# Kernel tuning notes

Hardware: AMD Instinct MI355X
Metric: run time of the kernel (lower is better)

The kernel has to match this reference:

```python
import jax, jax.numpy as jnp
import numpy as np

B, P = 4, 2048
N = B * P
QD = 512            # query_dim == inner_dim (pos_emb is added to raw features)
CD = 512            # context_dim
HEADS, DH = 8, 64
INNER = HEADS * DH
SCALE = DH ** -0.5
HC, WC = 32, 32     # context spatial grid
L = HC * WC         # context_len
SELF_HW = 512       # spatial_dim[:2]
STRIDE = 8          # resolution_level == sparse tensor stride
PE_H = SELF_HW // STRIDE  # 64 BEV pos-emb grid


def setup_inputs() -> dict:
    key = jax.random.key(0)
    k = jax.random.split(key, 9)
    return {
        "feats": jax.random.normal(k[0], (N, QD), jnp.float32),
        "coords_xy": jax.random.randint(k[1], (N, 2), 0, SELF_HW),
        "context_emb": jax.random.normal(k[2], (B, HC, WC, CD), jnp.float32),
        "Wq": jax.random.normal(k[3], (QD, INNER), jnp.float32) * 0.02,
        "Wk": jax.random.normal(k[4], (CD, INNER), jnp.float32) * 0.02,
        "Wv": jax.random.normal(k[5], (CD, INNER), jnp.float32) * 0.02,
        "Wo": jax.random.normal(k[6], (INNER, QD), jnp.float32) * 0.02,
        "bo": jnp.zeros((QD,), jnp.float32),
        "pos_embedding": jax.random.normal(k[7], (PE_H, PE_H, INNER), jnp.float32) / INNER ** 0.5,
        "context_pos_embedding": jax.random.normal(k[8], (L, CD), jnp.float32) / INNER ** 0.5,
    }


def _neighbor_mask(coords_xy):
    # get_context_mask: scatter a (2*STRIDE+1)^2 neighborhood around each point's
    # projected context cell into a [N, L] boolean mask
    ratio = jnp.float32(HC) / jnp.float32(SELF_HW)
    center = jnp.round(coords_xy.astype(jnp.float32) * ratio).astype(jnp.int32)  # [N,2]
    off = jnp.stack(
        jnp.meshgrid(jnp.arange(-STRIDE, STRIDE + 1), jnp.arange(-STRIDE, STRIDE + 1), indexing="ij"),
        axis=-1,
    ).reshape(-1, 2)  # [K,2], K = 289
    pos = center[:, None, :] + off[None, :, :]        # [N,K,2]
    r = jnp.clip(pos[..., 0], 0, HC - 1)
    c = jnp.clip(pos[..., 1], 0, WC - 1)
    flat = r * WC + c                                  # [N,K]
    return jnp.zeros((N, L), jnp.bool_).at[jnp.arange(N)[:, None], flat].set(True)


def reference(feats, coords_xy, context_emb, Wq, Wk, Wv, Wo, bo, pos_embedding, context_pos_embedding):
    # get_context: add learned context positional embedding, flatten spatial -> [B, L, CD]
    ctx = (context_emb + context_pos_embedding.reshape(HC, WC, CD)).reshape(B, L, CD)
    # get_pos_emb: gather BEV positional embedding per point via floor(coord/stride)
    rc = coords_xy // STRIDE                           # [N,2] in [0, 64)
    pe = pos_embedding[rc[:, 0], rc[:, 1]]             # [N, INNER]
    f = (feats + pe).reshape(B, P, QD)                 # points grouped per batch (equal counts)
    mask = _neighbor_mask(coords_xy).reshape(B, P, L)
    q = (f @ Wq).reshape(B, P, HEADS, DH).transpose(0, 2, 1, 3)    # [B,h,P,d]
    k = (ctx @ Wk).reshape(B, L, HEADS, DH).transpose(0, 2, 1, 3)  # [B,h,L,d]
    v = (ctx @ Wv).reshape(B, L, HEADS, DH).transpose(0, 2, 1, 3)
    sim = jnp.einsum("bhid,bhjd->bhij", q, k) * SCALE              # [B,h,P,L]
    neg = -jnp.finfo(sim.dtype).max
    sim = jnp.where(mask[:, None, :, :], sim, neg)
    attn = jax.nn.softmax(sim, axis=-1)
    out = jnp.einsum("bhij,bhjd->bhid", attn, v)
    out = out.transpose(0, 2, 1, 3).reshape(B, P, INNER)
    out = out @ Wo + bo                                # to_out (dropout=0, eval)
    return out.reshape(N, QD)                          # scatter back to point features
```

## Files before the change

### kernel.cpp

```cpp
#include <hip/hip_runtime.h>


typedef __attribute__((ext_vector_type(8))) short bf16x8;
typedef __attribute__((ext_vector_type(4))) float f32x4;

#define SCL 0.18033688f

__device__ __forceinline__ unsigned short f2bf(float x) {
  union { float f; unsigned int u; } v; v.f = x;
  unsigned int r = v.u + 0x7FFFu + ((v.u >> 16) & 1u);
  return (unsigned short)(r >> 16);
}

__device__ __forceinline__ unsigned int pk2bf(float a, float b) {
  return (unsigned)f2bf(a) | ((unsigned)f2bf(b) << 16);
}

__device__ __forceinline__ unsigned int cvtpk(float a, float b) {
  unsigned int r;
  asm("v_cvt_pk_bf16_f32 %0, %1, %2" : "=v"(r) : "v"(a), "v"(b));
  return r;
}

__device__ __forceinline__ float fexp2(float x) {
#if __has_builtin(__builtin_amdgcn_exp2f)
  return __builtin_amdgcn_exp2f(x);
#else
  return exp2f(x);
#endif
}

__device__ __forceinline__ int swzb(int row, int chk) {
  return row * 128 + ((chk * 16) ^ ((row & 7) << 4));
}

__global__ __launch_bounds__(256) void prep_w(const float* __restrict__ Wq, const float* __restrict__ Wk,
                                              const float* __restrict__ Wv, const float* __restrict__ Wo,
                                              unsigned short* __restrict__ Wqt, unsigned short* __restrict__ Wkt,
                                              unsigned short* __restrict__ Wvt, unsigned short* __restrict__ Wot) {
  __shared__ float tile[64][65];
  const int bid = blockIdx.x;
  const int wsel = bid >> 6, tt = bid & 63;
  const int kt = (tt >> 3) << 6, ntb = (tt & 7) << 6;
  const float* W = (wsel == 0) ? Wq : (wsel == 1) ? Wk : (wsel == 2) ? Wv : Wo;
  unsigned short* Wt = (wsel == 0) ? Wqt : (wsel == 1) ? Wkt : (wsel == 2) ? Wvt : Wot;
  const int t = threadIdx.x;
#pragma unroll
  for (int p = 0; p < 16; ++p) {
    int e = p * 256 + t;
    int row = e >> 6, col = e & 63;
    tile[row][col] = W[(long)(kt + row) * 512 + ntb + col];
  }
  __syncthreads();
#pragma unroll
  for (int p = 0; p < 16; ++p) {
    int e = p * 256 + t;
    int n = e >> 6, k = e & 63;
    Wt[(long)(ntb + n) * 512 + kt + k] = f2bf(tile[k][n]);
  }
}

__global__ __launch_bounds__(256) void prep_in(const float* __restrict__ feats,
                                               const int* __restrict__ coords,
                                               const float* __restrict__ pos_emb,
                                               const float* __restrict__ ctx,
                                               const float* __restrict__ ctx_pos,
                                               unsigned short* __restrict__ Aq,
                                               unsigned short* __restrict__ Ac) {
  int i = blockIdx.x * 256 + threadIdx.x;
  if (i < 1048576) {
    int e = i << 2;
    int q = e >> 9, k = e & 511;
    int pi = ((coords[2 * q] >> 3) << 6) + (coords[2 * q + 1] >> 3);
    float4 a = *(const float4*)(feats + e);
    float4 p = *(const float4*)(pos_emb + ((size_t)pi << 9) + k);
    uint2 o;
    o.x = pk2bf(a.x + p.x, a.y + p.y);
    o.y = pk2bf(a.z + p.z, a.w + p.w);
    *(uint2*)(Aq + e) = o;
  } else {
    int e = (i - 1048576) << 2;
    int r = e >> 9, k = e & 511;
    float4 a = *(const float4*)(ctx + e);
    float4 p = *(const float4*)(ctx_pos + ((size_t)(r & 1023) << 9) + k);
    uint2 o;
    o.x = pk2bf(a.x + p.x, a.y + p.y);
    o.y = pk2bf(a.z + p.z, a.w + p.w);
    *(uint2*)(Ac + e) = o;
  }
}

__global__ __launch_bounds__(256) void gemm_qkv(const unsigned short* __restrict__ Aq,
                                                const unsigned short* __restrict__ Ac,
                                                const unsigned short* __restrict__ Wqt,
                                                const unsigned short* __restrict__ Wkt,
                                                const unsigned short* __restrict__ Wvt,
                                                unsigned short* __restrict__ Qb,
                                                unsigned short* __restrict__ Kb,
                                                unsigned short* __restrict__ Vt) {
  __shared__ unsigned short As[128][72];
  __shared__ unsigned short Bs[128][72];
  const int t = threadIdx.x, l = t & 63, wid = t >> 6;
  const int wr = (wid >> 1) << 6, wc = (wid & 1) << 6;
  const int orig = blockIdx.x;
  const int bx = (orig & 7) * 64 + (orig >> 3);
  const bool isQ = bx < 256;
  long tm; const unsigned short* Bt; const unsigned short* Ab; bool isV = false; int nt;
  if (isQ) {
    tm = (long)(bx >> 2) * 128;
    nt = bx & 3;
    Bt = Wqt + (long)nt * 65536;
    Ab = Aq;
  } else {
    const int kvx = bx - 256;
    tm = (long)(kvx >> 3) * 128;
    const int y = kvx & 7;
    isV = y >= 4; nt = y & 3;
    Bt = (isV ? Wvt : Wkt) + (long)nt * 65536;
    Ab = Ac;
  }

  f32x4 acc[4][4] = {};
  const int lr = l & 15, lk = (l >> 4) << 3;
  const int srw = t >> 3, sch = (t & 7) << 3;

  for (int s = 0; s < 8; ++s) {
    const int k0 = s << 6;
    int4 rav[4], rbv[4];
#pragma unroll
    for (int p = 0; p < 4; ++p) {
      int row = srw + (p << 5);
      rav[p] = *(const int4*)(Ab + (tm + row) * 512 + k0 + sch);
      rbv[p] = *(const int4*)(Bt + (long)row * 512 + k0 + sch);
    }
#pragma unroll
    for (int p = 0; p < 4; ++p) {
      int row = srw + (p << 5);
      *(int4*)(&As[row][sch]) = rav[p];
      *(int4*)(&Bs[row][sch]) = rbv[p];
    }
    __syncthreads();
#pragma unroll
    for (int kk = 0; kk < 2; ++kk) {
      bf16x8 af[4], bfr[4];
#pragma unroll
      for (int i = 0; i < 4; ++i) af[i]  = *(const bf16x8*)(&As[wr + i * 16 + lr][kk * 32 + lk]);
#pragma unroll
      for (int i = 0; i < 4; ++i) bfr[i] = *(const bf16x8*)(&Bs[wc + i * 16 + lr][kk * 32 + lk]);
#pragma unroll
      for (int mi = 0; mi < 4; ++mi)
#pragma unroll
        for (int ni = 0; ni < 4; ++ni)
          acc[mi][ni] = __builtin_amdgcn_mfma_f32_16x16x32_bf16(af[mi], bfr[ni], acc[mi][ni], 0, 0, 0);
    }
    __syncthreads();
  }

  const int lq = (l >> 4) << 2;
#pragma unroll
  for (int mi = 0; mi < 4; ++mi)
#pragma unroll
    for (int ni = 0; ni < 4; ++ni) {
      int cn = nt * 128 + wc + ni * 16 + lr;
      long r0 = tm + wr + mi * 16 + lq;
      if (isQ) {
#pragma unroll
        for (int r = 0; r < 4; ++r)
          Qb[(r0 + r) * 512 + cn] = f2bf(acc[mi][ni][r] * SCL);
      } else if (!isV) {
#pragma unroll
        for (int r = 0; r < 4; ++r)
          Kb[(r0 + r) * 512 + cn] = f2bf(acc[mi][ni][r]);
      } else {
        int h = cn >> 6, d = cn & 63;
#pragma unroll
        for (int r = 0; r < 4; ++r) {
          long row = r0 + r;
          int b = (int)(row >> 10), j = (int)(row & 1023);
          int jp = (j & ~63) | ((j & 15) << 2) | ((j >> 4) & 3);
          Vt[((long)(b * 8 + h) * 64 + d) * 1024 + jp] = f2bf(acc[mi][ni][r]);
        }
      }
    }
}

__global__ __launch_bounds__(512, 4) void attn_mfma(const unsigned short* __restrict__ Qb,
                                                    const unsigned short* __restrict__ Kb,
                                                    const unsigned short* __restrict__ Vt,
                                                    const int* __restrict__ coords,
                                                    unsigned short* __restrict__ Abf) {
  __shared__ char Kl[2][8192];
  __shared__ char Vl[2][8192];
  __shared__ char Ol[2048];
  __shared__ unsigned short Plds[8][16][72];
  const int t = threadIdx.x, w = t >> 6, l = t & 63;
  const int g = l >> 4, lc = l & 15;
  const int orig = blockIdx.x;
  const int sw = (orig & 7) * 64 + (orig >> 3);
  const int qx = sw & 15, bh = sw >> 4;
  const int b = bh >> 3, h = bh & 7;
  const long qrow0 = (long)b * 2048 + qx * 128 + w * 16;

  int rm[4], cm[4];
#pragma unroll
  for (int r = 0; r < 4; ++r) {
    long qq = qrow0 + g * 4 + r;
    int cr = (int)rintf((float)coords[2 * qq] * 0.0625f);
    int cc = (int)rintf((float)coords[2 * qq + 1] * 0.0625f);
    int rlo = max(0, cr - 8), rhi = min(31, cr + 8);
    int clo = max(0, cc - 8), chi = min(31, cc + 8);
    rm[r] = (int)((((unsigned)1 << (rhi - rlo + 1)) - 1) << rlo);
    cm[r] = (int)((((unsigned)1 << (chi - clo + 1)) - 1) << clo);
  }

  bf16x8 qfr[2];
#pragma unroll
  for (int dc = 0; dc < 2; ++dc)
    qfr[dc] = *(const bf16x8*)(Qb + (qrow0 + lc) * 512 + h * 64 + dc * 32 + g * 8);

  const int srow = t >> 3, schk = t & 7;
  const unsigned short* Kg = Kb + ((long)b * 1024) * 512 + h * 64;
  const unsigned short* Vg = Vt + ((long)bh * 64) * 1024;

  if (t < 128) {
    int r = t >> 3, c = t & 7;
    unsigned short vv = (r == 0) ? (unsigned short)0x3F80 : (unsigned short)0;
    unsigned short tmp[8] = {vv, vv, vv, vv, vv, vv, vv, vv};
    *(int4*)(Ol + swzb(r, c)) = *(int4*)tmp;
  }
  {
    int4 sk = *(const int4*)(Kg + (long)srow * 512 + schk * 8);
    int4 sv_ = *(const int4*)(Vg + (long)srow * 1024 + schk * 8);
    *(int4*)(Kl[0] + swzb(srow, schk)) = sk;
    *(int4*)(Vl[0] + swzb(srow, schk)) = sv_;
  }
  __syncthreads();

  f32x4 po[5] = {};

  for (int kt = 0; kt < 16; ++kt) {
    const int cur = kt & 1;
    const int kb = kt * 64;
    int4 nk = {}, nv = {};
    if (kt < 15) {
      const int kbn = kb + 64;
      nk = *(const int4*)(Kg + (long)(kbn + srow) * 512 + schk * 8);
      nv = *(const int4*)(Vg + (long)srow * 1024 + kbn + schk * 8);
    }

    bf16x8 kfr[4][2];
#pragma unroll
    for (int kf = 0; kf < 4; ++kf)
#pragma unroll
      for (int dc = 0; dc < 2; ++dc)
        kfr[kf][dc] = *(const bf16x8*)(Kl[cur] + swzb(kf * 16 + lc, dc * 4 + g));

    f32x4 sv[4];
#pragma unroll
    for (int kf = 0; kf < 4; ++kf) {
      f32x4 a = {};
      a = __builtin_amdgcn_mfma_f32_16x16x32_bf16(qfr[0], kfr[kf][0], a, 0, 0, 0);
      a = __builtin_amdgcn_mfma_f32_16x16x32_bf16(qfr[1], kfr[kf][1], a, 0, 0, 0);
      sv[kf] = a;
    }

    const int jrb = kb >> 5;
    int cmk[4][4];
#pragma unroll
    for (int kf = 0; kf < 4; ++kf) {
      int jr = jrb + (kf >> 1);
#pragma unroll
      for (int r = 0; r < 4; ++r)
        cmk[kf][r] = ((rm[r] >> jr) & 1) ? cm[r] : 0;
    }
#pragma unroll
    for (int kf = 0; kf < 4; ++kf) {
      int jc = ((kf & 1) << 4) + lc;
#pragma unroll
      for (int r = 0; r < 4; ++r) {
        float p = fexp2(sv[kf][r]);
        sv[kf][r] = ((cmk[kf][r] >> jc) & 1) ? p : 0.0f;
      }
    }

    bf16x8 vfr[5][2];
#pragma unroll
    for (int df = 0; df < 4; ++df)
#pragma unroll
      for (int kc = 0; kc < 2; ++kc)
        vfr[df][kc] = *(const bf16x8*)(Vl[cur] + swzb(df * 16 + lc, kc * 4 + g));
#pragma unroll
    for (int kc = 0; kc < 2; ++kc)
      vfr[4][kc] = *(const bf16x8*)(Ol + swzb(lc, kc * 4 + g));

#pragma unroll
    for (int r = 0; r < 4; ++r) {
      uint2 pk;
      pk.x = cvtpk(sv[0][r], sv[1][r]);
      pk.y = cvtpk(sv[2][r], sv[3][r]);
      *(uint2*)(&Plds[w][g * 4 + r][4 * lc]) = pk;
    }

    bf16x8 pa0 = *(const bf16x8*)(&Plds[w][lc][g * 8]);
    bf16x8 pa1 = *(const bf16x8*)(&Plds[w][lc][32 + g * 8]);
    __builtin_amdgcn_s_setprio(1);
#pragma unroll
    for (int df = 0; df < 5; ++df) {
      po[df] = __builtin_amdgcn_mfma_f32_16x16x32_bf16(pa0, vfr[df][0], po[df], 0, 0, 0);
      po[df] = __builtin_amdgcn_mfma_f32_16x16x32_bf16(pa1, vfr[df][1], po[df], 0, 0, 0);
    }
    __builtin_amdgcn_s_setprio(0);

    if (kt < 15) {
      const int nxt = cur ^ 1;
      *(int4*)(Kl[nxt] + swzb(srow, schk)) = nk;
      *(int4*)(Vl[nxt] + swzb(srow, schk)) = nv;
    }
    __syncthreads();
  }

#pragma unroll
  for (int r = 0; r < 4; ++r) {
    float lsum = __shfl(po[4][r], l & 48);
    float inv = 1.0f / lsum;
    long qr = qrow0 + g * 4 + r;
#pragma unroll
    for (int df = 0; df < 4; ++df)
      Abf[qr * 512 + h * 64 + df * 16 + lc] = f2bf(po[df][r] * inv);
  }
}

__global__ __launch_bounds__(256) void gemm_o(const unsigned short* __restrict__ A,
                                              const unsigned short* __restrict__ Bt,
                                              float* __restrict__ C,
                                              const float* __restrict__ bias) {
  __shared__ unsigned short As[64][72];
  __shared__ unsigned short Bs[128][72];
  const int t = threadIdx.x, l = t & 63, wid = t >> 6;
  const int wr = (wid >> 1) << 5;
  const int wc = (wid & 1) << 6;
  const int orig = blockIdx.x;
  const int bx = (orig & 7) * 64 + (orig >> 3);
  const long tm = (long)(bx >> 2) * 64;
  const long tn = (long)(bx & 3) * 128;

  f32x4 acc[2][4] = {};
  const int lr = l & 15, lk = (l >> 4) << 3;
  for (int s = 0; s < 8; ++s) {
    const int k0 = s << 6;
    int4 rAv[2], rBv[4];
#pragma unroll
    for (int p = 0; p < 2; ++p) {
      int e = p * 256 + t;
      int row = e >> 3, ch = (e & 7) << 3;
      rAv[p] = *(const int4*)(A + (tm + row) * 512 + k0 + ch);
    }
#pragma unroll
    for (int p = 0; p < 4; ++p) {
      int e = p * 256 + t;
      int row = e >> 3, ch = (e & 7) << 3;
      rBv[p] = *(const int4*)(Bt + (tn + row) * 512 + k0 + ch);
    }
#pragma unroll
    for (int p = 0; p < 2; ++p) {
      int e = p * 256 + t;
      int row = e >> 3, ch = (e & 7) << 3;
      *(int4*)(&As[row][ch]) = rAv[p];
    }
#pragma unroll
    for (int p = 0; p < 4; ++p) {
      int e = p * 256 + t;
      int row = e >> 3, ch = (e & 7) << 3;
      *(int4*)(&Bs[row][ch]) = rBv[p];
    }
    __syncthreads();
#pragma unroll
    for (int kk = 0; kk < 2; ++kk) {
      bf16x8 af[2], bfr[4];
#pragma unroll
      for (int i = 0; i < 2; ++i) af[i]  = *(const bf16x8*)(&As[wr + i * 16 + lr][kk * 32 + lk]);
#pragma unroll
      for (int i = 0; i < 4; ++i) bfr[i] = *(const bf16x8*)(&Bs[wc + i * 16 + lr][kk * 32 + lk]);
#pragma unroll
      for (int mi = 0; mi < 2; ++mi)
#pragma unroll
        for (int ni = 0; ni < 4; ++ni)
          acc[mi][ni] = __builtin_amdgcn_mfma_f32_16x16x32_bf16(af[mi], bfr[ni], acc[mi][ni], 0, 0, 0);
    }
    __syncthreads();
  }

  const int lq = (l >> 4) << 2;
#pragma unroll
  for (int mi = 0; mi < 2; ++mi)
#pragma unroll
    for (int ni = 0; ni < 4; ++ni) {
      long col = tn + wc + ni * 16 + lr;
      float bv = bias[col];
      long r0 = tm + wr + mi * 16 + lq;
#pragma unroll
      for (int r = 0; r < 4; ++r)
        C[(r0 + r) * 512 + col] = acc[mi][ni][r] + bv;
    }
}

extern "C" void kernel_launch(void* const* d_in, const int* in_sizes, int n_in,
                              void* d_out, int out_size, void* d_ws, size_t ws_size,
                              hipStream_t stream) {
  (void)in_sizes; (void)n_in; (void)out_size; (void)ws_size;
  const float* feats   = (const float*)d_in[0];
  const int*   coords  = (const int*)d_in[1];
  const float* ctx     = (const float*)d_in[2];
  const float* Wq      = (const float*)d_in[3];
  const float* Wk      = (const float*)d_in[4];
  const float* Wv      = (const float*)d_in[5];
  const float* Wo      = (const float*)d_in[6];
  const float* bo      = (const float*)d_in[7];
  const float* pos_emb = (const float*)d_in[8];
  const float* ctx_pos = (const float*)d_in[9];
  float* out = (float*)d_out;
  char* ws = (char*)d_ws;

  unsigned short* Wqt = (unsigned short*)(ws);
  unsigned short* Wkt = (unsigned short*)(ws + 524288);
  unsigned short* Wvt = (unsigned short*)(ws + 1048576);
  unsigned short* Wot = (unsigned short*)(ws + 1572864);
  unsigned short* Aq  = (unsigned short*)(ws + 2097152);
  unsigned short* Ac  = (unsigned short*)(ws + 10485760);
  unsigned short* Qb  = (unsigned short*)(ws + 14680064);
  unsigned short* Kb  = (unsigned short*)(ws + 23068672);
  unsigned short* Vt  = (unsigned short*)(ws + 27262976);
  unsigned short* Abf = (unsigned short*)(ws + 31457280);

  prep_w  <<<256, 256, 0, stream>>>(Wq, Wk, Wv, Wo, Wqt, Wkt, Wvt, Wot);
  prep_in <<<6144, 256, 0, stream>>>(feats, coords, pos_emb, ctx, ctx_pos, Aq, Ac);
  gemm_qkv<<<512, 256, 0, stream>>>(Aq, Ac, Wqt, Wkt, Wvt, Qb, Kb, Vt);
  attn_mfma<<<512, 512, 0, stream>>>(Qb, Kb, Vt, coords, Abf);
  gemm_o  <<<512, 256, 0, stream>>>(Abf, Wot, out, bo);
}
```

Baseline: 96.07 us.

## Sort queries by context row and skip fully masked key tiles

Adds a per-batch counting sort of queries by their projected context row, computed in extra blocks of the input-prep kernel. The attention kernel then processes queries in sorted order. Each block reduces the min and max neighbourhood row over its queries and iterates only over the key tiles inside that row range. The aim is to avoid QK^T, softmax and PV work on tiles that the neighbourhood mask zeroes out anyway. The cost is indirect gathers of Q rows and coords, scattered output writes, and an extra sort pass.

```diff
diff --git a/kernel.cpp b/kernel.cpp
--- a/kernel.cpp
+++ b/kernel.cpp
@@ -66,7 +66,36 @@
                                                const float* __restrict__ ctx,
                                                const float* __restrict__ ctx_pos,
                                                unsigned short* __restrict__ Aq,
-                                               unsigned short* __restrict__ Ac) {
+                                               unsigned short* __restrict__ Ac,
+                                               int* __restrict__ perm) {
+  if (blockIdx.x >= 6144) {
+    __shared__ int hist[64];
+    __shared__ int base[64];
+    const int bb = blockIdx.x - 6144;
+    const int t = threadIdx.x;
+    if (t < 64) hist[t] = 0;
+    __syncthreads();
+    int keys[8];
+#pragma unroll
+    for (int i = 0; i < 8; ++i) {
+      int q = bb * 2048 + t * 8 + i;
+      int cr = (int)rintf((float)coords[2 * q] * 0.0625f);
+      keys[i] = cr;
+      atomicAdd(&hist[cr], 1);
+    }
+    __syncthreads();
+    if (t == 0) {
+      int s = 0;
+      for (int k2 = 0; k2 < 64; ++k2) { base[k2] = s; s += hist[k2]; }
+    }
+    __syncthreads();
+#pragma unroll
+    for (int i = 0; i < 8; ++i) {
+      int pos = atomicAdd(&base[keys[i]], 1);
+      perm[bb * 2048 + pos] = t * 8 + i;
+    }
+    return;
+  }
   int i = blockIdx.x * 256 + threadIdx.x;
   if (i < 1048576) {
     int e = i << 2;
@@ -188,35 +217,52 @@
                                                     const unsigned short* __restrict__ Kb,
                                                     const unsigned short* __restrict__ Vt,
                                                     const int* __restrict__ coords,
+                                                    const int* __restrict__ perm,
                                                     unsigned short* __restrict__ Abf) {
   __shared__ char Kl[2][8192];
   __shared__ char Vl[2][8192];
   __shared__ char Ol[2048];
   __shared__ unsigned short Plds[8][16][72];
+  __shared__ int permL[128];
+  __shared__ int rng[2];
   const int t = threadIdx.x, w = t >> 6, l = t & 63;
   const int g = l >> 4, lc = l & 15;
   const int orig = blockIdx.x;
   const int sw = (orig & 7) * 64 + (orig >> 3);
   const int qx = sw & 15, bh = sw >> 4;
   const int b = bh >> 3, h = bh & 7;
-  const long qrow0 = (long)b * 2048 + qx * 128 + w * 16;
+
+  if (t < 128) permL[t] = perm[b * 2048 + qx * 128 + t];
+  if (t == 0) { rng[0] = 63; rng[1] = 0; }
+  __syncthreads();
 
   int rm[4], cm[4];
+  int lrmin = 63, lrmax = 0;
 #pragma unroll
   for (int r = 0; r < 4; ++r) {
-    long qq = qrow0 + g * 4 + r;
+    long qq = (long)b * 2048 + permL[w * 16 + g * 4 + r];
     int cr = (int)rintf((float)coords[2 * qq] * 0.0625f);
     int cc = (int)rintf((float)coords[2 * qq + 1] * 0.0625f);
     int rlo = max(0, cr - 8), rhi = min(31, cr + 8);
     int clo = max(0, cc - 8), chi = min(31, cc + 8);
     rm[r] = (int)((((unsigned)1 << (rhi - rlo + 1)) - 1) << rlo);
     cm[r] = (int)((((unsigned)1 << (chi - clo + 1)) - 1) << clo);
-  }
+    lrmin = min(lrmin, rlo); lrmax = max(lrmax, rhi);
+  }
+#pragma unroll
+  for (int off = 32; off > 0; off >>= 1) {
+    lrmin = min(lrmin, __shfl_xor(lrmin, off));
+    lrmax = max(lrmax, __shfl_xor(lrmax, off));
+  }
+  if (l == 0) { atomicMin(&rng[0], lrmin); atomicMax(&rng[1], lrmax); }
 
   bf16x8 qfr[2];
-#pragma unroll
-  for (int dc = 0; dc < 2; ++dc)
-    qfr[dc] = *(const bf16x8*)(Qb + (qrow0 + lc) * 512 + h * 64 + dc * 32 + g * 8);
+  {
+    long qrow = (long)b * 2048 + permL[w * 16 + lc];
+#pragma unroll
+    for (int dc = 0; dc < 2; ++dc)
+      qfr[dc] = *(const bf16x8*)(Qb + qrow * 512 + h * 64 + dc * 32 + g * 8);
+  }
 
   const int srow = t >> 3, schk = t & 7;
   const unsigned short* Kg = Kb + ((long)b * 1024) * 512 + h * 64;
@@ -228,9 +274,12 @@
     unsigned short tmp[8] = {vv, vv, vv, vv, vv, vv, vv, vv};
     *(int4*)(Ol + swzb(r, c)) = *(int4*)tmp;
   }
+  __syncthreads();
+  const int t0 = rng[0] >> 1, t1 = rng[1] >> 1;
   {
-    int4 sk = *(const int4*)(Kg + (long)srow * 512 + schk * 8);
-    int4 sv_ = *(const int4*)(Vg + (long)srow * 1024 + schk * 8);
+    const int kb0 = t0 * 64;
+    int4 sk = *(const int4*)(Kg + (long)(kb0 + srow) * 512 + schk * 8);
+    int4 sv_ = *(const int4*)(Vg + (long)srow * 1024 + kb0 + schk * 8);
     *(int4*)(Kl[0] + swzb(srow, schk)) = sk;
     *(int4*)(Vl[0] + swzb(srow, schk)) = sv_;
   }
@@ -238,11 +287,11 @@
 
   f32x4 po[5] = {};
 
-  for (int kt = 0; kt < 16; ++kt) {
-    const int cur = kt & 1;
+  for (int kt = t0; kt <= t1; ++kt) {
+    const int cur = (kt - t0) & 1;
     const int kb = kt * 64;
     int4 nk = {}, nv = {};
-    if (kt < 15) {
+    if (kt < t1) {
       const int kbn = kb + 64;
       nk = *(const int4*)(Kg + (long)(kbn + srow) * 512 + schk * 8);
       nv = *(const int4*)(Vg + (long)srow * 1024 + kbn + schk * 8);
@@ -311,7 +360,7 @@
     }
     __builtin_amdgcn_s_setprio(0);
 
-    if (kt < 15) {
+    if (kt < t1) {
       const int nxt = cur ^ 1;
       *(int4*)(Kl[nxt] + swzb(srow, schk)) = nk;
       *(int4*)(Vl[nxt] + swzb(srow, schk)) = nv;
@@ -323,7 +372,7 @@
   for (int r = 0; r < 4; ++r) {
     float lsum = __shfl(po[4][r], l & 48);
     float inv = 1.0f / lsum;
-    long qr = qrow0 + g * 4 + r;
+    long qr = (long)b * 2048 + permL[w * 16 + g * 4 + r];
 #pragma unroll
     for (int df = 0; df < 4; ++df)
       Abf[qr * 512 + h * 64 + df * 16 + lc] = f2bf(po[df][r] * inv);
@@ -431,10 +480,11 @@
   unsigned short* Kb  = (unsigned short*)(ws + 23068672);
   unsigned short* Vt  = (unsigned short*)(ws + 27262976);
   unsigned short* Abf = (unsigned short*)(ws + 31457280);
+  int*            prm = (int*)(ws + 39845888);
 
   prep_w  <<<256, 256, 0, stream>>>(Wq, Wk, Wv, Wo, Wqt, Wkt, Wvt, Wot);
-  prep_in <<<6144, 256, 0, stream>>>(feats, coords, pos_emb, ctx, ctx_pos, Aq, Ac);
+  prep_in <<<6148, 256, 0, stream>>>(feats, coords, pos_emb, ctx, ctx_pos, Aq, Ac, prm);
   gemm_qkv<<<512, 256, 0, stream>>>(Aq, Ac, Wqt, Wkt, Wvt, Qb, Kb, Vt);
-  attn_mfma<<<512, 512, 0, stream>>>(Qb, Kb, Vt, coords, Abf);
+  attn_mfma<<<512, 512, 0, stream>>>(Qb, Kb, Vt, coords, prm, Abf);
   gemm_o  <<<512, 256, 0, stream>>>(Abf, Wot, out, bo);
 }
```

Result: faster. 91.79 us (-4.5%).
